# Kernel optimization log

Hardware: AMD Instinct MI355X
Metric: run time of the kernel (lower is better)

## Reference

```python
import jax, jax.numpy as jnp
import numpy as np

N, F, FE, NB = 50000, 64, 64, 16
E, T = 1_600_000, 1_000_000
IN_DIM = F + 2 * FE + NB  # 208
VAR = 0.15
EPS = 1e-5  # BatchNorm eps


def setup_inputs() -> dict:
    key = jax.random.key(0)
    ks = jax.random.split(key, 10)
    atom_fea = jax.random.normal(ks[0], (N, F), dtype=jnp.float32)
    edge_fea = jax.random.normal(ks[1], (E, FE), dtype=jnp.float32)
    r_ij = jax.random.normal(ks[2], (E, 3), dtype=jnp.float32)
    dist = jax.random.uniform(ks[3], (E,), dtype=jnp.float32, minval=0.5, maxval=5.0)
    cutoff_w = jax.random.uniform(ks[4], (E,), dtype=jnp.float32)
    fc_w = jax.random.normal(ks[5], (2 * F, IN_DIM), dtype=jnp.float32) / np.sqrt(IN_DIM)
    fc_b = jax.random.normal(ks[6], (2 * F,), dtype=jnp.float32) * 0.01
    bn1_gamma = jnp.ones((2 * F,), jnp.float32)
    bn1_beta = jnp.zeros((2 * F,), jnp.float32)
    bn2_gamma = jnp.ones((F,), jnp.float32)
    bn2_beta = jnp.zeros((F,), jnp.float32)
    edge_index = jax.random.randint(ks[7], (2, E), 0, N, dtype=jnp.int32)
    triplet_idx = jax.random.randint(ks[8], (2, T), 0, E, dtype=jnp.int32)
    return dict(atom_fea=atom_fea, edge_fea=edge_fea, r_ij=r_ij, dist=dist,
                cutoff_w=cutoff_w, fc_w=fc_w, fc_b=fc_b,
                bn1_gamma=bn1_gamma, bn1_beta=bn1_beta,
                bn2_gamma=bn2_gamma, bn2_beta=bn2_beta,
                edge_index=edge_index, triplet_idx=triplet_idx)


def _batchnorm(x, gamma, beta):
    # training-mode BatchNorm1d: biased batch statistics
    mu = x.mean(axis=0)
    var = ((x - mu) ** 2).mean(axis=0)
    return (x - mu) * jax.lax.rsqrt(var + EPS) * gamma + beta


def reference(atom_fea, edge_fea, r_ij, dist, cutoff_w, fc_w, fc_b,
              bn1_gamma, bn1_beta, bn2_gamma, bn2_beta,
              edge_index, triplet_idx):
    e1, e2 = triplet_idx[0], triplet_idx[1]
    dst = edge_index[1]
    # angle between neighbour displacement vectors
    v1 = r_ij[e1]            # (T,3)
    v2 = r_ij[e2]            # (T,3)
    d1 = jnp.maximum(dist[e1], 1e-8)
    d2 = jnp.maximum(dist[e2], 1e-8)
    cos_angle = jnp.clip((v1 * v2).sum(-1) / (d1 * d2), -1.0, 1.0)  # (T,)
    centers = jnp.linspace(-1.0, 1.0, NB)
    ang_fea = jnp.exp(-((cos_angle[:, None] - centers) ** 2) / (VAR ** 2))  # (T,NB)
    centre_atoms = dst[e1]   # (T,)
    triplet_fea = jnp.concatenate(
        [atom_fea[centre_atoms], edge_fea[e1], edge_fea[e2], ang_fea], axis=1)  # (T, IN_DIM)
    triplet_fea = _batchnorm(triplet_fea @ fc_w.T + fc_b, bn1_gamma, bn1_beta)  # (T, 2F)
    gate = jax.nn.sigmoid(triplet_fea[:, :F])
    core = jax.nn.softplus(triplet_fea[:, F:])
    messages = gate * core
    messages = messages * (cutoff_w[e1] * cutoff_w[e2])[:, None]
    aggr = jax.ops.segment_sum(messages, centre_atoms, num_segments=N)  # (N,F)
    aggr = _batchnorm(aggr, bn2_gamma, bn2_beta)
    return jax.nn.softplus(atom_fea + aggr)
```

## Files before the change

kernel.cpp:

```cpp
#include <hip/hip_runtime.h>
#include <hip/hip_bf16.h>
#include <math.h>

typedef __bf16 bf16;
typedef __bf16 bf16x8 __attribute__((ext_vector_type(8)));
typedef float  f32x4  __attribute__((ext_vector_type(4)));

#define MT     64
#define ROWPAD 232
#define NREP   32

union PK8 { bf16 h[8]; uint4 u; };

__device__ inline uint4 pack8(const float4 a, const float4 b) {
  PK8 p;
  p.h[0] = (bf16)a.x; p.h[1] = (bf16)a.y; p.h[2] = (bf16)a.z; p.h[3] = (bf16)a.w;
  p.h[4] = (bf16)b.x; p.h[5] = (bf16)b.y; p.h[6] = (bf16)b.z; p.h[7] = (bf16)b.w;
  return p.u;
}

__device__ inline bf16x8 zero_bf16x8() {
  PK8 z; z.u = make_uint4(0u, 0u, 0u, 0u);
  return *(bf16x8*)z.h;
}

__global__ __launch_bounds__(256)
void k_cvt(const float* __restrict__ src, bf16* __restrict__ dst, long n8) {
  const long i = (long)blockIdx.x * 256 + threadIdx.x;
  if (i >= n8) return;
  const float4* p = (const float4*)(src + i * 8);
  *(uint4*)(dst + i * 8) = pack8(p[0], p[1]);
}

__global__ __launch_bounds__(256)
void k_cvtw(const float* __restrict__ fc_w, bf16* __restrict__ dst) {
  const int i = blockIdx.x * 256 + threadIdx.x;
  if (i >= 128 * 28) return;
  const int row = i / 28, c = i - row * 28;
  uint4 v;
  if (c < 26) {
    const float4* p = (const float4*)(fc_w + (size_t)row * 208 + c * 8);
    v = pack8(p[0], p[1]);
  } else {
    v = make_uint4(0u, 0u, 0u, 0u);
  }
  *(uint4*)(dst + (size_t)row * 224 + c * 8) = v;
}

template<bool PRE>
__global__ __launch_bounds__(256)
void k_gemm(const float* __restrict__ atom_fea,
            const float* __restrict__ edge_fea,
            const bf16*  __restrict__ atom_bf,
            const bf16*  __restrict__ edge_bf,
            const float* __restrict__ r_ij,
            const float* __restrict__ dist,
            const float* __restrict__ cutoff_w,
            const float* __restrict__ fc_w,
            const bf16*  __restrict__ fcw_bf,
            const float* __restrict__ fc_b,
            const int*  __restrict__ eidx_dst,
            const int*  __restrict__ trip_e1,
            const int*  __restrict__ trip_e2,
            float* __restrict__ stat1,
            float* __restrict__ zbuf,
            int*   __restrict__ centre,
            float* __restrict__ cwbuf)
{
  __shared__ __align__(16) bf16 smA[MT * ROWPAD];

  const int tid  = threadIdx.x;
  const int lane = tid & 63;
  const int wv   = tid >> 6;
  const int quad = lane >> 4;
  const int l16  = lane & 15;
  const int t0   = blockIdx.x * MT;

  bf16x8 bfrag[2][7];
  float  bias_v[2];
#pragma unroll
  for (int ns = 0; ns < 2; ++ns) {
    const int col = wv * 32 + ns * 16 + l16;
    bias_v[ns] = fc_b[col];
#pragma unroll
    for (int kc = 0; kc < 7; ++kc) {
      if (PRE) {
        bfrag[ns][kc] = *(const bf16x8*)(fcw_bf + (size_t)col * 224 + kc * 32 + quad * 8);
      } else {
        const int k0 = kc * 32 + quad * 8;
        if (k0 < 208) {
          const float4* p = (const float4*)(fc_w + (size_t)col * 208 + k0);
          PK8 pk; pk.u = pack8(p[0], p[1]);
          bfrag[ns][kc] = *(bf16x8*)pk.h;
        } else {
          bfrag[ns][kc] = zero_bf16x8();
        }
      }
    }
  }

  if (PRE) {
    const int row = tid >> 2;
    const int cq  = tid & 3;
    const int t   = t0 + row;
    const int e1  = trip_e1[t];
    const int e2  = trip_e2[t];
    const int ca  = eidx_dst[e1];
    const bf16* ar = atom_bf + (size_t)ca * 64;
    const bf16* r1 = edge_bf + (size_t)e1 * 64;
    const bf16* r2 = edge_bf + (size_t)e2 * 64;
    const uint4 v0 = *(const uint4*)(ar + cq * 8);
    const uint4 v1 = *(const uint4*)(ar + (cq + 4) * 8);
    const uint4 v2 = *(const uint4*)(r1 + cq * 8);
    const uint4 v3 = *(const uint4*)(r1 + (cq + 4) * 8);
    const uint4 v4 = *(const uint4*)(r2 + cq * 8);
    const uint4 v5 = *(const uint4*)(r2 + (cq + 4) * 8);
    uint4 v6;
    if (cq < 2) {
      const float x1 = r_ij[e1 * 3], y1 = r_ij[e1 * 3 + 1], z1 = r_ij[e1 * 3 + 2];
      const float x2 = r_ij[e2 * 3], y2 = r_ij[e2 * 3 + 1], z2 = r_ij[e2 * 3 + 2];
      const float d1 = fmaxf(dist[e1], 1e-8f);
      const float d2 = fmaxf(dist[e2], 1e-8f);
      float cv = (x1 * x2 + y1 * y2 + z1 * z2) / (d1 * d2);
      cv = fminf(1.f, fmaxf(-1.f, cv));
      PK8 p;
      const int b0 = cq * 8;
#pragma unroll
      for (int j = 0; j < 8; ++j) {
        const float ctr = -1.f + (float)(b0 + j) * (2.f / 15.f);
        const float dd = cv - ctr;
        p.h[j] = (bf16)__expf(-(dd * dd) * 44.4444444f);
      }
      v6 = p.u;
    } else {
      v6 = make_uint4(0u, 0u, 0u, 0u);
    }
    if (cq == 0) {
      centre[t] = ca;
      cwbuf[t] = cutoff_w[e1] * cutoff_w[e2];
    }
    bf16* dstr = smA + row * ROWPAD;
    *(uint4*)(dstr + cq * 8)        = v0;
    *(uint4*)(dstr + (cq + 4) * 8)  = v1;
    *(uint4*)(dstr + (cq + 8) * 8)  = v2;
    *(uint4*)(dstr + (cq + 12) * 8) = v3;
    *(uint4*)(dstr + (cq + 16) * 8) = v4;
    *(uint4*)(dstr + (cq + 20) * 8) = v5;
    *(uint4*)(dstr + (cq + 24) * 8) = v6;
  } else {
    for (int i = tid; i < MT * 28; i += 256) {
      const int row = i / 28;
      const int c   = i - row * 28;
      const int t   = t0 + row;
      uint4 val;
      if (c < 8) {
        const int e1 = trip_e1[t];
        const int ca = eidx_dst[e1];
        const float4* p = (const float4*)(atom_fea + (size_t)ca * 64 + c * 8);
        val = pack8(p[0], p[1]);
        if (c == 0) {
          const int e2 = trip_e2[t];
          centre[t] = ca;
          cwbuf[t] = cutoff_w[e1] * cutoff_w[e2];
        }
      } else if (c < 16) {
        const int e1 = trip_e1[t];
        const float4* p = (const float4*)(edge_fea + (size_t)e1 * 64 + (c - 8) * 8);
        val = pack8(p[0], p[1]);
      } else if (c < 24) {
        const int e2 = trip_e2[t];
        const float4* p = (const float4*)(edge_fea + (size_t)e2 * 64 + (c - 16) * 8);
        val = pack8(p[0], p[1]);
      } else if (c < 26) {
        const int e1 = trip_e1[t];
        const int e2 = trip_e2[t];
        const float x1 = r_ij[e1 * 3], y1 = r_ij[e1 * 3 + 1], z1 = r_ij[e1 * 3 + 2];
        const float x2 = r_ij[e2 * 3], y2 = r_ij[e2 * 3 + 1], z2 = r_ij[e2 * 3 + 2];
        const float d1 = fmaxf(dist[e1], 1e-8f);
        const float d2 = fmaxf(dist[e2], 1e-8f);
        float cv = (x1 * x2 + y1 * y2 + z1 * z2) / (d1 * d2);
        cv = fminf(1.f, fmaxf(-1.f, cv));
        PK8 p;
        const int b0 = (c - 24) * 8;
#pragma unroll
        for (int j = 0; j < 8; ++j) {
          const float ctr = -1.f + (float)(b0 + j) * (2.f / 15.f);
          const float dd = cv - ctr;
          p.h[j] = (bf16)__expf(-(dd * dd) * 44.4444444f);
        }
        val = p.u;
      } else {
        val = make_uint4(0u, 0u, 0u, 0u);
      }
      *(uint4*)(smA + row * ROWPAD + c * 8) = val;
    }
  }
  __syncthreads();

  f32x4 acc[4][2] = {};
#pragma unroll
  for (int kc = 0; kc < 7; ++kc) {
    bf16x8 afr[4];
#pragma unroll
    for (int ms = 0; ms < 4; ++ms)
      afr[ms] = *(const bf16x8*)(smA + (ms * 16 + l16) * ROWPAD + kc * 32 + quad * 8);
#pragma unroll
    for (int ms = 0; ms < 4; ++ms)
#pragma unroll
      for (int ns = 0; ns < 2; ++ns)
        acc[ms][ns] = __builtin_amdgcn_mfma_f32_16x16x32_bf16(afr[ms], bfrag[ns][kc], acc[ms][ns], 0, 0, 0);
  }

  float* zr = zbuf + (size_t)t0 * 128;
#pragma unroll
  for (int ns = 0; ns < 2; ++ns) {
    const int col = wv * 32 + ns * 16 + l16;
    float s = 0.f, s2 = 0.f;
#pragma unroll
    for (int ms = 0; ms < 4; ++ms)
#pragma unroll
      for (int r = 0; r < 4; ++r) {
        const float zv = acc[ms][ns][r] + bias_v[ns];
        __builtin_nontemporal_store(zv, zr + (size_t)(ms * 16 + quad * 4 + r) * 128 + col);
        s += zv; s2 += zv * zv;
      }
    s  += __shfl_xor(s, 16);  s  += __shfl_xor(s, 32);
    s2 += __shfl_xor(s2, 16); s2 += __shfl_xor(s2, 32);
    if (quad == 0) {
      float* sb = stat1 + (size_t)(blockIdx.x & (NREP - 1)) * 256;
      atomicAdd(sb + col, s);
      atomicAdd(sb + 128 + col, s2);
    }
  }
}

__global__ void k_fin1(const float* __restrict__ stat1,
                       const float* __restrict__ g1, const float* __restrict__ b1,
                       float* __restrict__ bn1sc, float* __restrict__ bn1sh, float invT) {
  const int j = threadIdx.x;
  float s = 0.f, s2 = 0.f;
  for (int r = 0; r < NREP; ++r) { s += stat1[r * 256 + j]; s2 += stat1[r * 256 + 128 + j]; }
  const float mu  = s * invT;
  const float var = fmaxf(s2 * invT - mu * mu, 0.f);
  const float sc  = g1[j] * rsqrtf(var + 1e-5f);
  bn1sc[j] = sc;
  bn1sh[j] = b1[j] - mu * sc;
}

__global__ __launch_bounds__(256)
void k_apply(const float* __restrict__ zbuf,
             const int*   __restrict__ centre,
             const float* __restrict__ cwbuf,
             const float* __restrict__ bn1sc, const float* __restrict__ bn1sh,
             float* __restrict__ aggr, int T)
{
  const int lane = threadIdx.x & 63;
  const int sub  = threadIdx.x >> 6;
  const float scg = bn1sc[lane],      shg = bn1sh[lane];
  const float scc = bn1sc[64 + lane], shc = bn1sh[64 + lane];
  for (int t = blockIdx.x * 4 + sub; t < T; t += gridDim.x * 4) {
    const float zg = __builtin_nontemporal_load(zbuf + (size_t)t * 128 + lane)      * scg + shg;
    const float zc = __builtin_nontemporal_load(zbuf + (size_t)t * 128 + 64 + lane) * scc + shc;
    const float gate = 1.f / (1.f + __expf(-zg));
    const float core = (zc > 20.f) ? zc : log1pf(__expf(zc));
    atomicAdd(aggr + (size_t)centre[t] * 64 + lane, gate * core * cwbuf[t]);
  }
}

__global__ __launch_bounds__(256)
void k_bn2stats(const float* __restrict__ aggr, float* __restrict__ stat2, int N) {
  const int col = threadIdx.x & 63;
  const int rg  = threadIdx.x >> 6;
  float s = 0.f, s2 = 0.f;
  for (int n = blockIdx.x * 4 + rg; n < N; n += gridDim.x * 4) {
    const float v = aggr[(size_t)n * 64 + col];
    s += v; s2 += v * v;
  }
  __shared__ float ps[4][64], ps2[4][64];
  ps[rg][col] = s; ps2[rg][col] = s2;
  __syncthreads();
  if (rg == 0) {
    s  = ps[0][col] + ps[1][col] + ps[2][col] + ps[3][col];
    s2 = ps2[0][col] + ps2[1][col] + ps2[2][col] + ps2[3][col];
    atomicAdd(stat2 + col, s);
    atomicAdd(stat2 + 64 + col, s2);
  }
}

__global__ __launch_bounds__(256)
void k_final(const float* __restrict__ aggr, const float* __restrict__ atom,
             const float* __restrict__ stat2,
             const float* __restrict__ g2, const float* __restrict__ b2,
             float* __restrict__ out, int total, float invN) {
  const int idx = blockIdx.x * 256 + threadIdx.x;
  if (idx >= total) return;
  const int col = idx & 63;
  const float mu  = stat2[col] * invN;
  const float var = fmaxf(stat2[64 + col] * invN - mu * mu, 0.f);
  const float sc  = g2[col] * rsqrtf(var + 1e-5f);
  const float sh  = b2[col] - mu * sc;
  const float x   = aggr[idx] * sc + sh + atom[idx];
  out[idx] = (x > 20.f) ? x : log1pf(__expf(x));
}

extern "C" void kernel_launch(void* const* d_in, const int* in_sizes, int n_in,
                              void* d_out, int out_size, void* d_ws, size_t ws_size,
                              hipStream_t stream) {
  const float* atom_fea = (const float*)d_in[0];
  const float* edge_fea = (const float*)d_in[1];
  const float* r_ij     = (const float*)d_in[2];
  const float* dist     = (const float*)d_in[3];
  const float* cutoff_w = (const float*)d_in[4];
  const float* fc_w     = (const float*)d_in[5];
  const float* fc_b     = (const float*)d_in[6];
  const float* bn1g     = (const float*)d_in[7];
  const float* bn1b     = (const float*)d_in[8];
  const float* bn2g     = (const float*)d_in[9];
  const float* bn2b     = (const float*)d_in[10];
  const int*  eidx      = (const int*)d_in[11];
  const int*  tidx      = (const int*)d_in[12];

  const int N = in_sizes[0] / 64;
  const int E = in_sizes[3];
  const int T = in_sizes[12] / 2;

  size_t off = 0;
  char* base = (char*)d_ws;
  auto carve = [&](size_t bytes) -> void* {
    void* p = base + off;
    off += (bytes + 255) & ~(size_t)255;
    return p;
  };
  float* aggr    = (float*)carve((size_t)N * 64 * 4);
  float* stat1   = (float*)carve((size_t)NREP * 256 * 4);
  float* bn1sc   = (float*)carve(128 * 4);
  float* bn1sh   = (float*)carve(128 * 4);
  float* stat2   = (float*)carve(128 * 4);
  float* cwbuf   = (float*)carve((size_t)T * 4);
  int*   centre  = (int*)carve((size_t)T * 4);
  float* zbuf    = (float*)carve((size_t)T * 128 * 4);
  bf16*  edge_bf = (bf16*)carve((size_t)E * 64 * 2);
  bf16*  atom_bf = (bf16*)carve((size_t)N * 64 * 2);
  bf16*  fcw_bf  = (bf16*)carve((size_t)128 * 224 * 2);
  const bool pre = (off <= ws_size);

  hipMemsetAsync(aggr,  0, (size_t)N * 64 * sizeof(float), stream);
  hipMemsetAsync(stat1, 0, (size_t)NREP * 256 * sizeof(float), stream);
  hipMemsetAsync(stat2, 0, 128 * sizeof(float), stream);

  const int nblk = T / MT;
  if (pre) {
    const long e8 = (long)E * 64 / 8;
    const long a8 = (long)N * 64 / 8;
    k_cvt<<<(int)((e8 + 255) / 256), 256, 0, stream>>>(edge_fea, edge_bf, e8);
    k_cvt<<<(int)((a8 + 255) / 256), 256, 0, stream>>>(atom_fea, atom_bf, a8);
    k_cvtw<<<14, 256, 0, stream>>>(fc_w, fcw_bf);
    k_gemm<true><<<nblk, 256, 0, stream>>>(atom_fea, edge_fea, atom_bf, edge_bf,
                                           r_ij, dist, cutoff_w, fc_w, fcw_bf, fc_b,
                                           eidx + E, tidx, tidx + T,
                                           stat1, zbuf, centre, cwbuf);
  } else {
    k_gemm<false><<<nblk, 256, 0, stream>>>(atom_fea, edge_fea, atom_bf, edge_bf,
                                            r_ij, dist, cutoff_w, fc_w, fcw_bf, fc_b,
                                            eidx + E, tidx, tidx + T,
                                            stat1, zbuf, centre, cwbuf);
  }
  k_fin1<<<1, 128, 0, stream>>>(stat1, bn1g, bn1b, bn1sc, bn1sh, 1.0f / (float)T);
  k_apply<<<4096, 256, 0, stream>>>(zbuf, centre, cwbuf, bn1sc, bn1sh, aggr, T);
  k_bn2stats<<<256, 256, 0, stream>>>(aggr, stat2, N);
  const int total = N * 64;
  k_final<<<(total + 255) / 256, 256, 0, stream>>>(aggr, atom_fea, stat2, bn2g, bn2b,
                                                   (float*)d_out, total, 1.0f / (float)N);
}
```

Baseline: 1.234 ms.

## Store GEMM intermediate as packed fp16 and replicate scatter accumulator

The pre-BatchNorm GEMM output buffer is now stored as packed fp16 pairs instead of fp32, halving the large write and read of the T×128 intermediate. The apply kernel unpacks the halves. It scatters into two replicated aggr copies chosen by block parity to reduce atomic contention, and the copies are summed in the bn2 stats pass. Minor changes also use nontemporal loads in the conversion kernel and restructure the angle-feature fill so one lane computes all 16 bins. fp16 storage adds rounding error and could overflow for large pre-norm values.

```diff
diff --git a/kernel.cpp b/kernel.cpp
--- a/kernel.cpp
+++ b/kernel.cpp
@@ -5,12 +5,14 @@
 typedef __bf16 bf16;
 typedef __bf16 bf16x8 __attribute__((ext_vector_type(8)));
 typedef float  f32x4  __attribute__((ext_vector_type(4)));
+typedef float  f32x4e __attribute__((ext_vector_type(4)));
 
 #define MT     64
 #define ROWPAD 232
 #define NREP   32
 
 union PK8 { bf16 h[8]; uint4 u; };
+union PKH { _Float16 h[2]; unsigned int u; };
 
 __device__ inline uint4 pack8(const float4 a, const float4 b) {
   PK8 p;
@@ -28,8 +30,12 @@
 void k_cvt(const float* __restrict__ src, bf16* __restrict__ dst, long n8) {
   const long i = (long)blockIdx.x * 256 + threadIdx.x;
   if (i >= n8) return;
-  const float4* p = (const float4*)(src + i * 8);
-  *(uint4*)(dst + i * 8) = pack8(p[0], p[1]);
+  const f32x4e a = __builtin_nontemporal_load((const f32x4e*)(src + i * 8));
+  const f32x4e b = __builtin_nontemporal_load((const f32x4e*)(src + i * 8 + 4));
+  PK8 p;
+#pragma unroll
+  for (int j = 0; j < 4; ++j) { p.h[j] = (bf16)a[j]; p.h[4 + j] = (bf16)b[j]; }
+  *(uint4*)(dst + i * 8) = p.u;
 }
 
 __global__ __launch_bounds__(256)
@@ -63,7 +69,7 @@
             const int*  __restrict__ trip_e1,
             const int*  __restrict__ trip_e2,
             float* __restrict__ stat1,
-            float* __restrict__ zbuf,
+            unsigned int* __restrict__ zbuf,
             int*   __restrict__ centre,
             float* __restrict__ cwbuf)
 {
@@ -115,38 +121,37 @@
     const uint4 v3 = *(const uint4*)(r1 + (cq + 4) * 8);
     const uint4 v4 = *(const uint4*)(r2 + cq * 8);
     const uint4 v5 = *(const uint4*)(r2 + (cq + 4) * 8);
-    uint4 v6;
-    if (cq < 2) {
+    bf16* dstr = smA + row * ROWPAD;
+    if (cq == 0) {
       const float x1 = r_ij[e1 * 3], y1 = r_ij[e1 * 3 + 1], z1 = r_ij[e1 * 3 + 2];
       const float x2 = r_ij[e2 * 3], y2 = r_ij[e2 * 3 + 1], z2 = r_ij[e2 * 3 + 2];
       const float d1 = fmaxf(dist[e1], 1e-8f);
       const float d2 = fmaxf(dist[e2], 1e-8f);
       float cv = (x1 * x2 + y1 * y2 + z1 * z2) / (d1 * d2);
       cv = fminf(1.f, fmaxf(-1.f, cv));
-      PK8 p;
-      const int b0 = cq * 8;
+      PK8 pa, pb;
 #pragma unroll
       for (int j = 0; j < 8; ++j) {
-        const float ctr = -1.f + (float)(b0 + j) * (2.f / 15.f);
-        const float dd = cv - ctr;
-        p.h[j] = (bf16)__expf(-(dd * dd) * 44.4444444f);
+        const float ca0 = cv - (-1.f + (float)j * (2.f / 15.f));
+        const float ca1 = cv - (-1.f + (float)(j + 8) * (2.f / 15.f));
+        pa.h[j] = (bf16)__expf(-(ca0 * ca0) * 44.4444444f);
+        pb.h[j] = (bf16)__expf(-(ca1 * ca1) * 44.4444444f);
       }
-      v6 = p.u;
-    } else {
-      v6 = make_uint4(0u, 0u, 0u, 0u);
-    }
-    if (cq == 0) {
+      *(uint4*)(dstr + 24 * 8) = pa.u;
+      *(uint4*)(dstr + 25 * 8) = pb.u;
       centre[t] = ca;
       cwbuf[t] = cutoff_w[e1] * cutoff_w[e2];
+    } else if (cq == 2) {
+      *(uint4*)(dstr + 26 * 8) = make_uint4(0u, 0u, 0u, 0u);
+    } else if (cq == 3) {
+      *(uint4*)(dstr + 27 * 8) = make_uint4(0u, 0u, 0u, 0u);
     }
-    bf16* dstr = smA + row * ROWPAD;
     *(uint4*)(dstr + cq * 8)        = v0;
     *(uint4*)(dstr + (cq + 4) * 8)  = v1;
     *(uint4*)(dstr + (cq + 8) * 8)  = v2;
     *(uint4*)(dstr + (cq + 12) * 8) = v3;
     *(uint4*)(dstr + (cq + 16) * 8) = v4;
     *(uint4*)(dstr + (cq + 20) * 8) = v5;
-    *(uint4*)(dstr + (cq + 24) * 8) = v6;
   } else {
     for (int i = tid; i < MT * 28; i += 256) {
       const int row = i / 28;
@@ -211,26 +216,30 @@
         acc[ms][ns] = __builtin_amdgcn_mfma_f32_16x16x32_bf16(afr[ms], bfrag[ns][kc], acc[ms][ns], 0, 0, 0);
   }
 
-  float* zr = zbuf + (size_t)t0 * 128;
-#pragma unroll
-  for (int ns = 0; ns < 2; ++ns) {
-    const int col = wv * 32 + ns * 16 + l16;
-    float s = 0.f, s2 = 0.f;
-#pragma unroll
-    for (int ms = 0; ms < 4; ++ms)
-#pragma unroll
-      for (int r = 0; r < 4; ++r) {
-        const float zv = acc[ms][ns][r] + bias_v[ns];
-        __builtin_nontemporal_store(zv, zr + (size_t)(ms * 16 + quad * 4 + r) * 128 + col);
-        s += zv; s2 += zv * zv;
-      }
-    s  += __shfl_xor(s, 16);  s  += __shfl_xor(s, 32);
-    s2 += __shfl_xor(s2, 16); s2 += __shfl_xor(s2, 32);
-    if (quad == 0) {
-      float* sb = stat1 + (size_t)(blockIdx.x & (NREP - 1)) * 256;
-      atomicAdd(sb + col, s);
-      atomicAdd(sb + 128 + col, s2);
+  unsigned int* zw = zbuf + (size_t)t0 * 64;
+  float s0 = 0.f, s20 = 0.f, s1 = 0.f, s21 = 0.f;
+#pragma unroll
+  for (int ms = 0; ms < 4; ++ms)
+#pragma unroll
+    for (int r = 0; r < 4; ++r) {
+      const float z0 = acc[ms][0][r] + bias_v[0];
+      const float z1 = acc[ms][1][r] + bias_v[1];
+      PKH pk; pk.h[0] = (_Float16)z0; pk.h[1] = (_Float16)z1;
+      const int row = ms * 16 + quad * 4 + r;
+      __builtin_nontemporal_store(pk.u, zw + (size_t)row * 64 + wv * 16 + l16);
+      s0 += z0; s20 += z0 * z0; s1 += z1; s21 += z1 * z1;
     }
+  s0  += __shfl_xor(s0, 16);  s0  += __shfl_xor(s0, 32);
+  s20 += __shfl_xor(s20, 16); s20 += __shfl_xor(s20, 32);
+  s1  += __shfl_xor(s1, 16);  s1  += __shfl_xor(s1, 32);
+  s21 += __shfl_xor(s21, 16); s21 += __shfl_xor(s21, 32);
+  if (quad == 0) {
+    float* sb = stat1 + (size_t)(blockIdx.x & (NREP - 1)) * 256;
+    const int c0 = wv * 32 + l16;
+    atomicAdd(sb + c0, s0);
+    atomicAdd(sb + 128 + c0, s20);
+    atomicAdd(sb + c0 + 16, s1);
+    atomicAdd(sb + 128 + c0 + 16, s21);
   }
 }
 
@@ -248,32 +257,41 @@
 }
 
 __global__ __launch_bounds__(256)
-void k_apply(const float* __restrict__ zbuf,
+void k_apply(const unsigned int* __restrict__ zbuf,
              const int*   __restrict__ centre,
              const float* __restrict__ cwbuf,
              const float* __restrict__ bn1sc, const float* __restrict__ bn1sh,
-             float* __restrict__ aggr, int T)
+             float* __restrict__ aggr, size_t repN, int T)
 {
   const int lane = threadIdx.x & 63;
   const int sub  = threadIdx.x >> 6;
-  const float scg = bn1sc[lane],      shg = bn1sh[lane];
-  const float scc = bn1sc[64 + lane], shc = bn1sh[64 + lane];
+  const int f    = lane;
+  const int wg   = ((f >> 5) << 4) | (f & 15);
+  const int sel  = (f >> 4) & 1;
+  const float scg = bn1sc[f],      shg = bn1sh[f];
+  const float scc = bn1sc[64 + f], shc = bn1sh[64 + f];
+  float* ag = aggr + (size_t)(blockIdx.x & 1) * repN;
   for (int t = blockIdx.x * 4 + sub; t < T; t += gridDim.x * 4) {
-    const float zg = __builtin_nontemporal_load(zbuf + (size_t)t * 128 + lane)      * scg + shg;
-    const float zc = __builtin_nontemporal_load(zbuf + (size_t)t * 128 + 64 + lane) * scc + shc;
+    const unsigned int ug = __builtin_nontemporal_load(zbuf + (size_t)t * 64 + wg);
+    const unsigned int uc = __builtin_nontemporal_load(zbuf + (size_t)t * 64 + 32 + wg);
+    PKH a, b; a.u = ug; b.u = uc;
+    const float zg = (sel ? (float)a.h[1] : (float)a.h[0]) * scg + shg;
+    const float zc = (sel ? (float)b.h[1] : (float)b.h[0]) * scc + shc;
     const float gate = 1.f / (1.f + __expf(-zg));
     const float core = (zc > 20.f) ? zc : log1pf(__expf(zc));
-    atomicAdd(aggr + (size_t)centre[t] * 64 + lane, gate * core * cwbuf[t]);
-  }
-}
-
-__global__ __launch_bounds__(256)
-void k_bn2stats(const float* __restrict__ aggr, float* __restrict__ stat2, int N) {
+    atomicAdd(ag + (size_t)centre[t] * 64 + f, gate * core * cwbuf[t]);
+  }
+}
+
+__global__ __launch_bounds__(256)
+void k_bn2stats(float* __restrict__ aggr, size_t repN, float* __restrict__ stat2, int N) {
   const int col = threadIdx.x & 63;
   const int rg  = threadIdx.x >> 6;
   float s = 0.f, s2 = 0.f;
   for (int n = blockIdx.x * 4 + rg; n < N; n += gridDim.x * 4) {
-    const float v = aggr[(size_t)n * 64 + col];
+    const size_t idx = (size_t)n * 64 + col;
+    const float v = aggr[idx] + aggr[repN + idx];
+    aggr[idx] = v;
     s += v; s2 += v * v;
   }
   __shared__ float ps[4][64], ps2[4][64];
@@ -324,6 +342,8 @@
   const int E = in_sizes[3];
   const int T = in_sizes[12] / 2;
 
+  const size_t repN = (size_t)N * 64;
+
   size_t off = 0;
   char* base = (char*)d_ws;
   auto carve = [&](size_t bytes) -> void* {
@@ -331,20 +351,20 @@
     off += (bytes + 255) & ~(size_t)255;
     return p;
   };
-  float* aggr    = (float*)carve((size_t)N * 64 * 4);
+  float* aggr    = (float*)carve(2 * repN * 4);
   float* stat1   = (float*)carve((size_t)NREP * 256 * 4);
   float* bn1sc   = (float*)carve(128 * 4);
   float* bn1sh   = (float*)carve(128 * 4);
   float* stat2   = (float*)carve(128 * 4);
   float* cwbuf   = (float*)carve((size_t)T * 4);
   int*   centre  = (int*)carve((size_t)T * 4);
-  float* zbuf    = (float*)carve((size_t)T * 128 * 4);
+  unsigned int* zbuf = (unsigned int*)carve((size_t)T * 64 * 4);
   bf16*  edge_bf = (bf16*)carve((size_t)E * 64 * 2);
   bf16*  atom_bf = (bf16*)carve((size_t)N * 64 * 2);
   bf16*  fcw_bf  = (bf16*)carve((size_t)128 * 224 * 2);
   const bool pre = (off <= ws_size);
 
-  hipMemsetAsync(aggr,  0, (size_t)N * 64 * sizeof(float), stream);
+  hipMemsetAsync(aggr,  0, 2 * repN * sizeof(float), stream);
   hipMemsetAsync(stat1, 0, (size_t)NREP * 256 * sizeof(float), stream);
   hipMemsetAsync(stat2, 0, 128 * sizeof(float), stream);
 
@@ -366,8 +386,8 @@
                                             stat1, zbuf, centre, cwbuf);
   }
   k_fin1<<<1, 128, 0, stream>>>(stat1, bn1g, bn1b, bn1sc, bn1sh, 1.0f / (float)T);
-  k_apply<<<4096, 256, 0, stream>>>(zbuf, centre, cwbuf, bn1sc, bn1sh, aggr, T);
-  k_bn2stats<<<256, 256, 0, stream>>>(aggr, stat2, N);
+  k_apply<<<4096, 256, 0, stream>>>(zbuf, centre, cwbuf, bn1sc, bn1sh, aggr, repN, T);
+  k_bn2stats<<<256, 256, 0, stream>>>(aggr, repN, stat2, N);
   const int total = N * 64;
   k_final<<<(total + 255) / 256, 256, 0, stream>>>(aggr, atom_fea, stat2, bn2g, bn2b,
                                                    (float*)d_out, total, 1.0f / (float)N);
```

After: 1.099 ms. 10.9% less time.
